# Optimization experiments

Hardware: AMD Instinct MI355X
Metric: run time of the kernel (lower is better)

## Reference

```python
import jax, jax.numpy as jnp
import numpy as np

B, N, DIM, H = 16, 1024, 512, 8
HEAD_DIM = DIM // H
SCALE = HEAD_DIM ** -0.5


def _dct_matrix(m):
    # Orthonormal DCT-II matrix, matching cv2.dct: D[0,:]=sqrt(1/m),
    # D[k,n]=sqrt(2/m)*cos(pi*(2n+1)*k/(2m)) for k>0.
    n = jnp.arange(m, dtype=jnp.float32)
    k = n[:, None]
    D = jnp.sqrt(2.0 / m) * jnp.cos(jnp.pi * (2.0 * n[None, :] + 1.0) * k / (2.0 * m))
    return D.at[0, :].set(jnp.sqrt(1.0 / m))


def setup_inputs() -> dict:
    key = jax.random.key(0)
    ks = jax.random.split(key, 9)
    def lin(k, fan_in, shape):
        return jax.random.normal(k, shape, jnp.float32) * (1.0 / np.sqrt(fan_in))
    return {
        "x": jax.random.normal(ks[0], (B, N, DIM), jnp.float32),
        "qkv_w": lin(ks[1], DIM, (DIM, 3 * DIM)),
        "qkv_b": lin(ks[2], DIM, (3 * DIM,)),
        "proj_w": lin(ks[3], DIM, (DIM, DIM)),
        "proj_b": lin(ks[4], DIM, (DIM,)),
        "h1_w": lin(ks[5], DIM, (DIM, DIM // 4)),
        "h1_b": jnp.zeros((DIM // 4,), jnp.float32),
        "h2_w": lin(ks[6], DIM // 4, (DIM // 4, H)),
        "h2_b": jnp.zeros((H,), jnp.float32),
        "freq_w": jnp.float32(0.5),
    }


def _extract_dct_features(x):
    # x: (B, N, C). Mirrors extract_dct_features incl. the .detach() in torch.
    B_, N_, _ = x.shape
    m = int(np.ceil(np.sqrt(N_)))  # static
    x_mean = x.mean(axis=-1)                                   # (B, N)
    A = jnp.pad(x_mean, ((0, 0), (0, m * m - N_))).reshape(B_, m, m)
    D = _dct_matrix(m)
    dct2 = jnp.einsum('km,bmn,ln->bkl', D, A, D)               # 2D DCT per sample
    dct_feat = dct2.reshape(B_, m * m)[:, :N_]
    dct_feat = jnp.clip(dct_feat, -10.0, 10.0)
    norm = jnp.linalg.norm(dct_feat, axis=1, keepdims=True) + 1e-5
    return jax.lax.stop_gradient(dct_feat / norm)              # (B, N)


def reference(x, qkv_w, qkv_b, proj_w, proj_b, h1_w, h1_b, h2_w, h2_b, freq_w):
    B_, N_, C = x.shape
    # QKV projection -> (3, B, H, N, head_dim)
    qkv = (x @ qkv_w + qkv_b).reshape(B_, N_, 3, H, C // H)
    qkv = jnp.transpose(qkv, (2, 0, 3, 1, 4))
    q, k, v = qkv[0] * SCALE, qkv[1], qkv[2]
    attn = jnp.einsum('bhnd,bhmd->bhnm', q, k)                 # (B, H, N, N)

    # Frequency-domain attention term
    dct_feat = _extract_dct_features(x)                        # (B, N)
    x_avg = x.mean(axis=1)                                     # (B, C)
    head_w = jax.nn.relu(x_avg @ h1_w + h1_b) @ h2_w + h2_b    # (B, H)
    weighted = dct_feat[:, None, :] * head_w[:, :, None]       # (B, H, N)
    freq_attn = jnp.einsum('bhn,bhm->bnm', weighted, weighted) # (B, N, N)
    row_sum = jnp.maximum(freq_attn.sum(axis=-1, keepdims=True), 1e-5)
    freq_attn = jnp.clip(freq_attn / row_sum, 0.0, 1.0)

    aw = jax.nn.sigmoid(freq_w)
    attn = (1.0 - aw) * attn + aw * freq_attn[:, None, :, :]
    attn = jax.nn.softmax(attn, axis=-1)

    out = jnp.einsum('bhnm,bhmd->bhnd', attn, v)
    out = jnp.transpose(out, (0, 2, 1, 3)).reshape(B_, N_, C)
    return out @ proj_w + proj_b
```

## Files before the change

### kernel.cpp

```cpp
#include <hip/hip_runtime.h>
#include <hip/hip_bf16.h>
#include <math.h>

#define PI_F  3.14159265358979323846f
#define LOG2E 1.44269504088896340736f

typedef __attribute__((ext_vector_type(8))) short          bf16x8;
typedef __attribute__((ext_vector_type(8))) unsigned short ushort8;
typedef __attribute__((ext_vector_type(4))) float          f32x4;

__device__ __forceinline__ unsigned short f2bf(float f) {
  union { float f; unsigned u; } v; v.f = f;
  unsigned r = v.u + 0x7fffu + ((v.u >> 16) & 1u);
  return (unsigned short)(r >> 16);
}

__device__ __forceinline__ unsigned short f2bf_hw(float f) {
  __hip_bfloat16 h = __float2bfloat16(f);
  return *reinterpret_cast<unsigned short*>(&h);
}

#define GLOAD16(g, l)                                                         \
  __builtin_amdgcn_global_load_lds(                                           \
      (const __attribute__((address_space(1))) void*)(g),                     \
      (__attribute__((address_space(3))) void*)(l), 16, 0, 0)

static const size_t OFF_XB  = 0;
static const size_t OFF_QB  = 16777216;
static const size_t OFF_KB  = 33554432;
static const size_t OFF_VT  = 67108864;
static const size_t OFF_AO  = 83886080;
static const size_t OFF_WT  = 100663296;
static const size_t OFF_PWT = 102236160;
static const size_t OFF_XM  = 102760448;
static const size_t OFF_XA  = 102825984;
static const size_t OFF_DF  = 102858752;
static const size_t OFF_CR  = 102924352;

__global__ __launch_bounds__(256) void k_xmean_cvt(const float* __restrict__ x,
                                                   float* __restrict__ xmean,
                                                   unsigned short* __restrict__ xb) {
  int row  = blockIdx.x * 4 + (threadIdx.x >> 6);
  int lane = threadIdx.x & 63;
  const float* px = x + (size_t)row * 512 + lane * 8;
  float4 a = ((const float4*)px)[0];
  float4 b = ((const float4*)px)[1];
  ushort8 o;
  o[0] = f2bf(a.x); o[1] = f2bf(a.y); o[2] = f2bf(a.z); o[3] = f2bf(a.w);
  o[4] = f2bf(b.x); o[5] = f2bf(b.y); o[6] = f2bf(b.z); o[7] = f2bf(b.w);
  *(ushort8*)(xb + (size_t)row * 512 + lane * 8) = o;
  float s = a.x + a.y + a.z + a.w + b.x + b.y + b.z + b.w;
  for (int off = 32; off; off >>= 1) s += __shfl_down(s, off);
  if (lane == 0) xmean[row] = s * (1.f / 512.f);
}

__global__ __launch_bounds__(512) void k_xavg(const unsigned short* __restrict__ xb,
                                              float* __restrict__ xavg) {
  int b = blockIdx.x, chunk = blockIdx.y;
  int c = threadIdx.x;
  const unsigned short* px = xb + ((size_t)b * 1024 + (size_t)chunk * 64) * 512 + c;
  float s = 0.f;
#pragma unroll 8
  for (int n = 0; n < 64; ++n) {
    unsigned u = (unsigned)px[(size_t)n * 512] << 16;
    s += *reinterpret_cast<float*>(&u);
  }
  atomicAdd(&xavg[b * 512 + c], s);
}

__global__ __launch_bounds__(1024) void k_dct_headw(const float* __restrict__ xmean,
                                                    const float* __restrict__ xavg,
                                                    const float* __restrict__ h1w,
                                                    const float* __restrict__ h1b,
                                                    const float* __restrict__ h2w,
                                                    const float* __restrict__ h2b,
                                                    const float* __restrict__ freqw,
                                                    float* __restrict__ dfeat,
                                                    float* __restrict__ crow) {
  __shared__ float A[32][33], Dm[32][33], Tm[32][33];
  __shared__ float red[1024];
  __shared__ float nrm, tsum_s;
  __shared__ float xa[512];
  __shared__ float part[8][128];
  __shared__ float h1s[128];
  __shared__ float hw[8];
  int b = blockIdx.x, t = threadIdx.x;
  if (t < 512) xa[t] = xavg[b * 512 + t] * (1.f / 1024.f);
  int kk = t >> 5, nn = t & 31;
  A[kk][nn] = xmean[b * 1024 + t];
  float dv = (kk == 0) ? sqrtf(1.f / 32.f)
                       : sqrtf(2.f / 32.f) * cosf(PI_F * (2.f * nn + 1.f) * (float)kk / 64.f);
  Dm[kk][nn] = dv;
  __syncthreads();
  float acc = 0.f;
  for (int m = 0; m < 32; ++m) acc += Dm[kk][m] * A[m][nn];
  Tm[kk][nn] = acc;
  __syncthreads();
  float acc2 = 0.f;
  for (int n = 0; n < 32; ++n) acc2 += Tm[kk][n] * Dm[nn][n];
  float val = fminf(fmaxf(acc2, -10.f), 10.f);
  red[t] = val * val;
  __syncthreads();
  for (int s = 512; s; s >>= 1) { if (t < s) red[t] += red[t + s]; __syncthreads(); }
  if (t == 0) nrm = sqrtf(red[0]) + 1e-5f;
  __syncthreads();
  float dn = val / nrm;
  dfeat[b * 1024 + t] = dn;
  red[t] = dn;
  __syncthreads();
  for (int s = 512; s; s >>= 1) { if (t < s) red[t] += red[t + s]; __syncthreads(); }
  if (t == 0) tsum_s = red[0];
  {
    int j = t & 127, c = t >> 7;
    float a1 = 0.f;
    const float* wcol = h1w + (size_t)c * 64 * 128 + j;
#pragma unroll 8
    for (int i = 0; i < 64; ++i) a1 += xa[c * 64 + i] * wcol[(size_t)i * 128];
    part[c][j] = a1;
  }
  __syncthreads();
  if (t < 128) {
    float a1 = h1b[t];
#pragma unroll
    for (int c = 0; c < 8; ++c) a1 += part[c][t];
    h1s[t] = fmaxf(a1, 0.f);
  }
  __syncthreads();
  if (t < 8) {
    float a2 = h2b[t];
    for (int j = 0; j < 128; ++j) a2 += h1s[j] * h2w[j * 8 + t];
    hw[t] = a2;
  }
  __syncthreads();
  float s2 = 0.f;
#pragma unroll
  for (int h = 0; h < 8; ++h) s2 += hw[h] * hw[h];
  float Tb = tsum_s;
  const float aw2 = (1.f / (1.f + __expf(-freqw[0]))) * LOG2E;
  float p = s2 * dn;
  crow[b * 1024 + t] = aw2 * p / fmaxf(p * Tb, 1e-5f);
}

__global__ __launch_bounds__(256) void k_wtrans2(const float* __restrict__ w1,
                                                 unsigned short* __restrict__ wt1,
                                                 const float* __restrict__ w2,
                                                 unsigned short* __restrict__ wt2) {
  __shared__ unsigned short T[64 * 65];
  int bx = blockIdx.x;
  const float* w;
  unsigned short* wt;
  int Nw, n0;
  if (bx < 24) { w = w1; wt = wt1; Nw = 1536; n0 = bx * 64; }
  else         { w = w2; wt = wt2; Nw = 512;  n0 = (bx - 24) * 64; }
  int k0 = blockIdx.y * 64;
  int t = threadIdx.x;
  int r = t >> 2, c0 = (t & 3) * 16;
  const float* src = w + (size_t)(k0 + r) * Nw + n0 + c0;
#pragma unroll
  for (int q = 0; q < 4; ++q) {
    float4 v4 = *(const float4*)(src + q * 4);
    T[(c0 + q * 4 + 0) * 65 + r] = f2bf(v4.x);
    T[(c0 + q * 4 + 1) * 65 + r] = f2bf(v4.y);
    T[(c0 + q * 4 + 2) * 65 + r] = f2bf(v4.z);
    T[(c0 + q * 4 + 3) * 65 + r] = f2bf(v4.w);
  }
  __syncthreads();
  int nl = t >> 2, koff = (t & 3) * 16;
  ushort8 o0, o1;
#pragma unroll
  for (int e = 0; e < 8; ++e) o0[e] = T[nl * 65 + koff + e];
#pragma unroll
  for (int e = 0; e < 8; ++e) o1[e] = T[nl * 65 + koff + 8 + e];
  unsigned short* dst = wt + (size_t)(n0 + nl) * 512 + k0 + koff;
  *(ushort8*)(dst) = o0;
  *(ushort8*)(dst + 8) = o1;
}

template <int MODE>
__global__ __launch_bounds__(256) void k_gemm(const unsigned short* __restrict__ A,
                                              const unsigned short* __restrict__ Bt,
                                              const float* __restrict__ bias,
                                              const float* __restrict__ freqw,
                                              unsigned short* __restrict__ o_q,
                                              unsigned short* __restrict__ o_k,
                                              unsigned short* __restrict__ o_vt,
                                              float* __restrict__ o_f) {
  __shared__ __align__(16) unsigned short As[128 * 64];
  __shared__ __align__(16) unsigned short Bs[128 * 64];
  const int t = threadIdx.x, w = t >> 6, l = t & 63;
  const int lg = l >> 4, ln = l & 15;
  const int wm = w >> 1, wn = w & 1;
  constexpr int NX = (MODE == 0) ? 12 : 4;
  const int bid = blockIdx.x, xcd = bid & 7, idx = bid >> 3;
  const int bx = idx % NX, by = xcd * 16 + idx / NX;
  const int row0 = by * 128, col0 = bx * 128;

  f32x4 acc[4][4];
#pragma unroll
  for (int i = 0; i < 4; ++i)
#pragma unroll
    for (int j = 0; j < 4; ++j) acc[i][j] = (f32x4){0.f, 0.f, 0.f, 0.f};

  int aoff[4][2], boff[4][2];
#pragma unroll
  for (int mt = 0; mt < 4; ++mt)
#pragma unroll
    for (int ks = 0; ks < 2; ++ks) {
      int ra = wm * 64 + mt * 16 + ln;
      aoff[mt][ks] = ra * 64 + (((lg + ks * 4) ^ (ra & 7)) << 3);
      int rb = wn * 64 + mt * 16 + ln;
      boff[mt][ks] = rb * 64 + (((lg + ks * 4) ^ (rb & 7)) << 3);
    }

  for (int k0 = 0; k0 < 512; k0 += 64) {
#pragma unroll
    for (int j = 0; j < 4; ++j) {
      int g = (j * 4 + w) * 64 + l;
      int row = g >> 3, slot = g & 7;
      int ss = slot ^ (row & 7);
      GLOAD16(A + (size_t)(row0 + row) * 512 + k0 + ss * 8, As + (size_t)(j * 4 + w) * 512);
      GLOAD16(Bt + (size_t)(col0 + row) * 512 + k0 + ss * 8, Bs + (size_t)(j * 4 + w) * 512);
    }
    __syncthreads();
#pragma unroll
    for (int ks = 0; ks < 2; ++ks) {
      bf16x8 av[4], bv[4];
#pragma unroll
      for (int mt = 0; mt < 4; ++mt) av[mt] = *(const bf16x8*)(As + aoff[mt][ks]);
#pragma unroll
      for (int nt = 0; nt < 4; ++nt) bv[nt] = *(const bf16x8*)(Bs + boff[nt][ks]);
#pragma unroll
      for (int mt = 0; mt < 4; ++mt)
#pragma unroll
        for (int nt = 0; nt < 4; ++nt)
          acc[mt][nt] = __builtin_amdgcn_mfma_f32_16x16x32_bf16(av[mt], bv[nt], acc[mt][nt], 0, 0, 0);
    }
    __syncthreads();
  }

  if (MODE == 0) {
    const int sel = col0 >> 9;
    if (sel == 2) {
      unsigned short* T = (wn == 0) ? As : Bs;
#pragma unroll
      for (int nt = 0; nt < 4; ++nt) {
        int dcol = nt * 16 + ln;
        float bcol = bias[col0 + wn * 64 + dcol];
#pragma unroll
        for (int mt = 0; mt < 4; ++mt)
#pragma unroll
          for (int r = 0; r < 4; ++r) {
            int rowL = wm * 64 + mt * 16 + lg * 4 + r;
            int slot = (rowL >> 3) ^ (dcol & 7);
            T[dcol * 128 + slot * 8 + (rowL & 7)] = f2bf(acc[mt][nt][r] + bcol);
          }
      }
      __syncthreads();
      int b_ = row0 >> 10, n0 = row0 & 1023;
      int h0 = (col0 & 511) >> 6;
      int dcol = t >> 2, rseg = (t & 3) * 32;
#pragma unroll
      for (int half = 0; half < 2; ++half) {
        const unsigned short* S = half ? Bs : As;
        size_t plane = ((size_t)(b_ * 8 + h0 + half)) << 16;
        unsigned short* dst = o_vt + plane + (size_t)dcol * 1024 + n0 + rseg;
#pragma unroll
        for (int j = 0; j < 4; ++j) {
          int slot = ((rseg >> 3) + j) ^ (dcol & 7);
          *(ushort8*)(dst + j * 8) = *(const ushort8*)(S + dcol * 128 + slot * 8);
        }
      }
      return;
    }
    unsigned short* outp = (sel == 0) ? o_q : o_k;
    const float aw = 1.f / (1.f + __expf(-freqw[0]));
    const float scl = (sel == 0) ? 0.125f * (1.f - aw) * LOG2E : 1.f;
#pragma unroll
    for (int nt = 0; nt < 4; ++nt) {
      int colg = col0 + wn * 64 + nt * 16 + ln;
      float bcol = bias[colg];
      int h = (colg >> 6) & 7, d = colg & 63;
#pragma unroll
      for (int mt = 0; mt < 4; ++mt)
#pragma unroll
        for (int r = 0; r < 4; ++r) {
          int row = row0 + wm * 64 + mt * 16 + lg * 4 + r;
          int bidx = row >> 10, n = row & 1023;
          float val = (acc[mt][nt][r] + bcol) * scl;
          outp[(((size_t)(bidx * 8 + h)) << 16) + (n << 6) + d] = f2bf(val);
        }
    }
  } else {
#pragma unroll
    for (int nt = 0; nt < 4; ++nt) {
      int colg = col0 + wn * 64 + nt * 16 + ln;
      float bcol = bias[colg];
#pragma unroll
      for (int mt = 0; mt < 4; ++mt)
#pragma unroll
        for (int r = 0; r < 4; ++r) {
          int row = row0 + wm * 64 + mt * 16 + lg * 4 + r;
          o_f[(size_t)row * 512 + colg] = acc[mt][nt][r] + bcol;
        }
    }
  }
}

__global__ __launch_bounds__(256) void k_attn(const unsigned short* __restrict__ qb,
                                              const unsigned short* __restrict__ kb,
                                              const unsigned short* __restrict__ vtg,
                                              const float* __restrict__ crow,
                                              const float* __restrict__ dfeat,
                                              const float* __restrict__ freqw,
                                              unsigned short* __restrict__ ao) {
  __shared__ __align__(16) unsigned short Ks[64 * 64];
  __shared__ __align__(16) unsigned short Vs[64 * 64];
  __shared__ __align__(16) unsigned short Ps[4][32 * 64];
  __shared__ __align__(16) float Df[1024];
  const int bid = blockIdx.x, xcd = bid & 7, idx = bid >> 3;
  const int bh = xcd * 16 + (idx >> 3), qt = idx & 7;
  const int b = bh >> 3, h = bh & 7;
  const int t = threadIdx.x, w = t >> 6, l = t & 63;
  const int lg = l >> 4, ln = l & 15;
  const size_t base = ((size_t)(b * 8 + h)) << 16;
  const float aw2 = (1.f / (1.f + __expf(-freqw[0]))) * LOG2E;

  *(float4*)(&Df[t * 4]) = *(const float4*)(dfeat + b * 1024 + t * 4);

  const int qrow0 = qt * 128 + w * 32;
  bf16x8 qf[2][2];
#pragma unroll
  for (int mt = 0; mt < 2; ++mt)
#pragma unroll
    for (int ks = 0; ks < 2; ++ks)
      qf[mt][ks] = *(const bf16x8*)(qb + base + (size_t)(qrow0 + mt * 16 + ln) * 64 + lg * 8 + ks * 32);

  float cr2[2][4];
#pragma unroll
  for (int mt = 0; mt < 2; ++mt)
#pragma unroll
    for (int r = 0; r < 4; ++r)
      cr2[mt][r] = crow[b * 1024 + qrow0 + mt * 16 + lg * 4 + r];

  f32x4 accO[2][4];
#pragma unroll
  for (int mt = 0; mt < 2; ++mt)
#pragma unroll
    for (int dt = 0; dt < 4; ++dt) accO[mt][dt] = (f32x4){0.f, 0.f, 0.f, 0.f};
  float mrow[2][4], psum[2][4];
#pragma unroll
  for (int mt = 0; mt < 2; ++mt)
#pragma unroll
    for (int r = 0; r < 4; ++r) { mrow[mt][r] = -1e30f; psum[mt][r] = 0.f; }

  int rdoff[2];
#pragma unroll
  for (int ks = 0; ks < 2; ++ks) rdoff[ks] = ln * 64 + (((lg + ks * 4) ^ (ln & 7)) << 3);
  int pwoff[4][4];
#pragma unroll
  for (int nt = 0; nt < 4; ++nt)
#pragma unroll
    for (int r = 0; r < 4; ++r) {
      int prow = lg * 4 + r;
      pwoff[nt][r] = prow * 64 + ((((nt << 1) | (ln >> 3)) ^ (prow & 7)) << 3) + (ln & 7);
    }

  for (int kt = 0; kt < 16; ++kt) {
    __syncthreads();
#pragma unroll
    for (int j = 0; j < 2; ++j) {
      int g = (j * 4 + w) * 64 + l;
      int row = g >> 3, slot = g & 7;
      int ss = slot ^ (row & 7);
      GLOAD16(kb + base + (size_t)(kt * 64 + row) * 64 + ss * 8, Ks + (size_t)(j * 4 + w) * 512);
      GLOAD16(vtg + base + (size_t)row * 1024 + kt * 64 + ss * 8, Vs + (size_t)(j * 4 + w) * 512);
    }
    __syncthreads();

    float dmv[4];
#pragma unroll
    for (int nt = 0; nt < 4; ++nt) dmv[nt] = Df[kt * 64 + nt * 16 + ln];
    f32x4 s[2][4];
#pragma unroll
    for (int mt = 0; mt < 2; ++mt)
#pragma unroll
      for (int nt = 0; nt < 4; ++nt)
#pragma unroll
        for (int r = 0; r < 4; ++r)
          s[mt][nt][r] = __builtin_amdgcn_fmed3f(cr2[mt][r] * dmv[nt], 0.f, aw2);
    __builtin_amdgcn_s_setprio(1);
#pragma unroll
    for (int nt = 0; nt < 4; ++nt) {
      bf16x8 kf0 = *(const bf16x8*)(Ks + nt * 1024 + rdoff[0]);
      bf16x8 kf1 = *(const bf16x8*)(Ks + nt * 1024 + rdoff[1]);
#pragma unroll
      for (int mt = 0; mt < 2; ++mt) {
        s[mt][nt] = __builtin_amdgcn_mfma_f32_16x16x32_bf16(qf[mt][0], kf0, s[mt][nt], 0, 0, 0);
        s[mt][nt] = __builtin_amdgcn_mfma_f32_16x16x32_bf16(qf[mt][1], kf1, s[mt][nt], 0, 0, 0);
      }
    }
    __builtin_amdgcn_s_setprio(0);

    float lmax[2][4];
    bool viol = false;
#pragma unroll
    for (int mt = 0; mt < 2; ++mt)
#pragma unroll
      for (int r = 0; r < 4; ++r) {
        lmax[mt][r] = fmaxf(fmaxf(s[mt][0][r], s[mt][1][r]), fmaxf(s[mt][2][r], s[mt][3][r]));
        viol = viol || (lmax[mt][r] > mrow[mt][r] + 8.f);
      }
    if (__any(viol)) {
#pragma unroll
      for (int mt = 0; mt < 2; ++mt)
#pragma unroll
        for (int r = 0; r < 4; ++r) {
          float pmax = lmax[mt][r];
          pmax = fmaxf(pmax, __shfl_xor(pmax, 1));
          pmax = fmaxf(pmax, __shfl_xor(pmax, 2));
          pmax = fmaxf(pmax, __shfl_xor(pmax, 4));
          pmax = fmaxf(pmax, __shfl_xor(pmax, 8));
          float mnew = fmaxf(mrow[mt][r], pmax);
          float sc = __builtin_amdgcn_exp2f(mrow[mt][r] - mnew);
          psum[mt][r] *= sc;
          mrow[mt][r] = mnew;
#pragma unroll
          for (int dt = 0; dt < 4; ++dt) accO[mt][dt][r] *= sc;
        }
    }
#pragma unroll
    for (int mt = 0; mt < 2; ++mt)
#pragma unroll
      for (int r = 0; r < 4; ++r) {
        float p0 = __builtin_amdgcn_exp2f(s[mt][0][r] - mrow[mt][r]);
        float p1 = __builtin_amdgcn_exp2f(s[mt][1][r] - mrow[mt][r]);
        float p2 = __builtin_amdgcn_exp2f(s[mt][2][r] - mrow[mt][r]);
        float p3 = __builtin_amdgcn_exp2f(s[mt][3][r] - mrow[mt][r]);
        psum[mt][r] += (p0 + p1) + (p2 + p3);
        Ps[w][mt * 1024 + pwoff[0][r]] = f2bf_hw(p0);
        Ps[w][mt * 1024 + pwoff[1][r]] = f2bf_hw(p1);
        Ps[w][mt * 1024 + pwoff[2][r]] = f2bf_hw(p2);
        Ps[w][mt * 1024 + pwoff[3][r]] = f2bf_hw(p3);
      }

    bf16x8 pa[2][2];
#pragma unroll
    for (int mt = 0; mt < 2; ++mt)
#pragma unroll
      for (int ks = 0; ks < 2; ++ks)
        pa[mt][ks] = *(const bf16x8*)(Ps[w] + mt * 1024 + rdoff[ks]);
    __builtin_amdgcn_s_setprio(1);
#pragma unroll
    for (int dt = 0; dt < 4; ++dt) {
      bf16x8 vf0 = *(const bf16x8*)(Vs + dt * 1024 + rdoff[0]);
      bf16x8 vf1 = *(const bf16x8*)(Vs + dt * 1024 + rdoff[1]);
#pragma unroll
      for (int mt = 0; mt < 2; ++mt) {
        accO[mt][dt] = __builtin_amdgcn_mfma_f32_16x16x32_bf16(pa[mt][0], vf0, accO[mt][dt], 0, 0, 0);
        accO[mt][dt] = __builtin_amdgcn_mfma_f32_16x16x32_bf16(pa[mt][1], vf1, accO[mt][dt], 0, 0, 0);
      }
    }
    __builtin_amdgcn_s_setprio(0);
  }

#pragma unroll
  for (int mt = 0; mt < 2; ++mt)
#pragma unroll
    for (int r = 0; r < 4; ++r) {
      float lr = psum[mt][r];
      lr += __shfl_xor(lr, 1);
      lr += __shfl_xor(lr, 2);
      lr += __shfl_xor(lr, 4);
      lr += __shfl_xor(lr, 8);
      float inv = 1.f / lr;
      int n = qrow0 + mt * 16 + lg * 4 + r;
#pragma unroll
      for (int dt = 0; dt < 4; ++dt)
        ao[((size_t)(b * 1024 + n)) * 512 + h * 64 + dt * 16 + ln] = f2bf(accO[mt][dt][r] * inv);
    }
}

extern "C" void kernel_launch(void* const* d_in, const int* in_sizes, int n_in,
                              void* d_out, int out_size, void* d_ws, size_t ws_size,
                              hipStream_t stream) {
  const float* x      = (const float*)d_in[0];
  const float* qkv_w  = (const float*)d_in[1];
  const float* qkv_b  = (const float*)d_in[2];
  const float* proj_w = (const float*)d_in[3];
  const float* proj_b = (const float*)d_in[4];
  const float* h1_w   = (const float*)d_in[5];
  const float* h1_b   = (const float*)d_in[6];
  const float* h2_w   = (const float*)d_in[7];
  const float* h2_b   = (const float*)d_in[8];
  const float* freq_w = (const float*)d_in[9];

  char* ws = (char*)d_ws;
  unsigned short* xb  = (unsigned short*)(ws + OFF_XB);
  unsigned short* qbp = (unsigned short*)(ws + OFF_QB);
  unsigned short* kbp = (unsigned short*)(ws + OFF_KB);
  unsigned short* vtg = (unsigned short*)(ws + OFF_VT);
  unsigned short* ao  = (unsigned short*)(ws + OFF_AO);
  unsigned short* wt  = (unsigned short*)(ws + OFF_WT);
  unsigned short* pwt = (unsigned short*)(ws + OFF_PWT);
  float* xmean = (float*)(ws + OFF_XM);
  float* xavg  = (float*)(ws + OFF_XA);
  float* dfeat = (float*)(ws + OFF_DF);
  float* crow  = (float*)(ws + OFF_CR);
  float* out   = (float*)d_out;

  hipMemsetAsync(xavg, 0, 16 * 512 * sizeof(float), stream);

  k_xmean_cvt<<<dim3(4096), 256, 0, stream>>>(x, xmean, xb);
  k_xavg<<<dim3(16, 16), 512, 0, stream>>>(xb, xavg);
  k_wtrans2<<<dim3(32, 8), 256, 0, stream>>>(qkv_w, wt, proj_w, pwt);
  k_dct_headw<<<dim3(16), 1024, 0, stream>>>(xmean, xavg, h1_w, h1_b, h2_w, h2_b,
                                             freq_w, dfeat, crow);
  k_gemm<0><<<dim3(12 * 128), 256, 0, stream>>>(xb, wt, qkv_b, freq_w, qbp, kbp, vtg, nullptr);
  k_attn<<<dim3(1024), 256, 0, stream>>>(qbp, kbp, vtg, crow, dfeat, freq_w, ao);
  k_gemm<1><<<dim3(4 * 128), 256, 0, stream>>>(ao, pwt, proj_b, freq_w, nullptr, nullptr, nullptr, out);
}
```

Before: 171.4 us.

## Double-buffer K/V tiles in attention kernel to overlap loads with compute

Changes the attention kernel's K and V shared-memory tiles to two buffers. The next tile is prefetched with global_load_lds while the current tile is computed, and the explicit __syncthreads pairs are replaced by manual waitcnt plus barrier. This aims to hide global load latency behind the MFMA and softmax work. It doubles the K/V LDS footprint, which may reduce occupancy, and depends on correct vmcnt accounting.

```diff
diff --git a/kernel.cpp b/kernel.cpp
--- a/kernel.cpp
+++ b/kernel.cpp
@@ -313,8 +313,8 @@
                                               const float* __restrict__ dfeat,
                                               const float* __restrict__ freqw,
                                               unsigned short* __restrict__ ao) {
-  __shared__ __align__(16) unsigned short Ks[64 * 64];
-  __shared__ __align__(16) unsigned short Vs[64 * 64];
+  __shared__ __align__(16) unsigned short Ks[2][64 * 64];
+  __shared__ __align__(16) unsigned short Vs[2][64 * 64];
   __shared__ __align__(16) unsigned short Ps[4][32 * 64];
   __shared__ __align__(16) float Df[1024];
   const int bid = blockIdx.x, xcd = bid & 7, idx = bid >> 3;
@@ -365,17 +365,30 @@
       pwoff[nt][r] = prow * 64 + ((((nt << 1) | (ln >> 3)) ^ (prow & 7)) << 3) + (ln & 7);
     }
 
+  const int g0 = w * 64 + l, g1 = (4 + w) * 64 + l;
+  const int srow0 = g0 >> 3, sslot0 = (g0 & 7) ^ (srow0 & 7);
+  const int srow1 = g1 >> 3, sslot1 = (g1 & 7) ^ (srow1 & 7);
+
+  GLOAD16(kb + base + (size_t)srow0 * 64 + sslot0 * 8, Ks[0] + (size_t)w * 512);
+  GLOAD16(vtg + base + (size_t)srow0 * 1024 + sslot0 * 8, Vs[0] + (size_t)w * 512);
+  GLOAD16(kb + base + (size_t)srow1 * 64 + sslot1 * 8, Ks[0] + (size_t)(4 + w) * 512);
+  GLOAD16(vtg + base + (size_t)srow1 * 1024 + sslot1 * 8, Vs[0] + (size_t)(4 + w) * 512);
+
   for (int kt = 0; kt < 16; ++kt) {
-    __syncthreads();
-#pragma unroll
-    for (int j = 0; j < 2; ++j) {
-      int g = (j * 4 + w) * 64 + l;
-      int row = g >> 3, slot = g & 7;
-      int ss = slot ^ (row & 7);
-      GLOAD16(kb + base + (size_t)(kt * 64 + row) * 64 + ss * 8, Ks + (size_t)(j * 4 + w) * 512);
-      GLOAD16(vtg + base + (size_t)row * 1024 + kt * 64 + ss * 8, Vs + (size_t)(j * 4 + w) * 512);
-    }
-    __syncthreads();
+    const int cur = kt & 1;
+    asm volatile("s_waitcnt lgkmcnt(0)" ::: "memory");
+    __builtin_amdgcn_s_barrier();
+    if (kt < 15) {
+      const int kn = kt + 1;
+      GLOAD16(kb + base + (size_t)(kn * 64 + srow0) * 64 + sslot0 * 8, Ks[cur ^ 1] + (size_t)w * 512);
+      GLOAD16(vtg + base + (size_t)srow0 * 1024 + kn * 64 + sslot0 * 8, Vs[cur ^ 1] + (size_t)w * 512);
+      GLOAD16(kb + base + (size_t)(kn * 64 + srow1) * 64 + sslot1 * 8, Ks[cur ^ 1] + (size_t)(4 + w) * 512);
+      GLOAD16(vtg + base + (size_t)srow1 * 1024 + kn * 64 + sslot1 * 8, Vs[cur ^ 1] + (size_t)(4 + w) * 512);
+      asm volatile("s_waitcnt vmcnt(4)" ::: "memory");
+    } else {
+      asm volatile("s_waitcnt vmcnt(0)" ::: "memory");
+    }
+    __builtin_amdgcn_s_barrier();
 
     float dmv[4];
 #pragma unroll
@@ -391,8 +404,8 @@
     __builtin_amdgcn_s_setprio(1);
 #pragma unroll
     for (int nt = 0; nt < 4; ++nt) {
-      bf16x8 kf0 = *(const bf16x8*)(Ks + nt * 1024 + rdoff[0]);
-      bf16x8 kf1 = *(const bf16x8*)(Ks + nt * 1024 + rdoff[1]);
+      bf16x8 kf0 = *(const bf16x8*)(Ks[cur] + nt * 1024 + rdoff[0]);
+      bf16x8 kf1 = *(const bf16x8*)(Ks[cur] + nt * 1024 + rdoff[1]);
 #pragma unroll
       for (int mt = 0; mt < 2; ++mt) {
         s[mt][nt] = __builtin_amdgcn_mfma_f32_16x16x32_bf16(qf[mt][0], kf0, s[mt][nt], 0, 0, 0);
@@ -452,8 +465,8 @@
     __builtin_amdgcn_s_setprio(1);
 #pragma unroll
     for (int dt = 0; dt < 4; ++dt) {
-      bf16x8 vf0 = *(const bf16x8*)(Vs + dt * 1024 + rdoff[0]);
-      bf16x8 vf1 = *(const bf16x8*)(Vs + dt * 1024 + rdoff[1]);
+      bf16x8 vf0 = *(const bf16x8*)(Vs[cur] + dt * 1024 + rdoff[0]);
+      bf16x8 vf1 = *(const bf16x8*)(Vs[cur] + dt * 1024 + rdoff[1]);
 #pragma unroll
       for (int mt = 0; mt < 2; ++mt) {
         accO[mt][dt] = __builtin_amdgcn_mfma_f32_16x16x32_bf16(pa[mt][0], vf0, accO[mt][dt], 0, 0, 0);
```

New measurement: 167.9 us (median of 2 runs). 1.02x faster.
